# Optimization experiments

Hardware: AMD Instinct MI355X
Metric: run time of the kernel (lower is better)

## Reference

```python
import jax, jax.numpy as jnp
import numpy as np

B, P, O, C = 64, 8732, 32, 81
IMG = 224.0
THRESH = 0.5
NEG_POS = 3.0
ALPHA = 1.0


def cxcy_to_xy(b):
    return jnp.concatenate([b[..., :2] - b[..., 2:] / 2, b[..., :2] + b[..., 2:] / 2], -1)


def xy_to_cxcy(b):
    return jnp.concatenate([(b[..., :2] + b[..., 2:]) / 2, b[..., 2:] - b[..., :2]], -1)


def coco_to_xy(b):  # [x, y, w, h] -> [xmin, ymin, xmax, ymax]
    return jnp.concatenate([b[..., :2], b[..., :2] + b[..., 2:]], -1)


def cxcy_to_gcxgcy(cxcy, priors):  # SSD offset encoding, variances 10 / 5
    g_cxcy = (cxcy[..., :2] - priors[..., :2]) / (priors[..., 2:] / 10.0)
    g_wh = jnp.log(cxcy[..., 2:] / priors[..., 2:]) * 5.0
    return jnp.concatenate([g_cxcy, g_wh], -1)


def pairwise_iou(a, b):  # a: [O,4] xy, b: [P,4] xy -> [O,P]
    lt = jnp.maximum(a[:, None, :2], b[None, :, :2])
    rb = jnp.minimum(a[:, None, 2:], b[None, :, 2:])
    wh = jnp.clip(rb - lt, 0.0)
    inter = wh[..., 0] * wh[..., 1]
    area_a = (a[:, 2] - a[:, 0]) * (a[:, 3] - a[:, 1])
    area_b = (b[:, 2] - b[:, 0]) * (b[:, 3] - b[:, 1])
    return inter / (area_a[:, None] + area_b[None, :] - inter)


def setup_inputs() -> dict:
    key = jax.random.key(0)
    k1, k2, k3, k4, k5, k6, k7 = jax.random.split(key, 7)
    pred_locs = jax.random.normal(k1, (B, P, 4), dtype=jnp.float32)
    pred_scores = jax.random.normal(k2, (B, P, C), dtype=jnp.float32)
    # COCO-format gt boxes [x, y, w, h] in pixel coords, guaranteed inside image
    xy = jax.random.uniform(k3, (B, O, 2), minval=0.0, maxval=IMG * 0.55)
    wh = jax.random.uniform(k4, (B, O, 2), minval=8.0, maxval=IMG * 0.4)
    gt_boxes = jnp.concatenate([xy, wh], -1)
    gt_labels = jax.random.randint(k5, (B, O), 1, C)  # foreground labels 1..C-1
    p_cxcy = jax.random.uniform(k6, (P, 2), minval=0.05, maxval=0.95)
    p_wh = jax.random.uniform(k7, (P, 2), minval=0.05, maxval=0.5)
    priors_cxcy = jnp.concatenate([p_cxcy, p_wh], -1)
    return {"pred_locs": pred_locs, "pred_scores": pred_scores,
            "gt_boxes": gt_boxes, "gt_labels": gt_labels,
            "priors_cxcy": priors_cxcy}


def reference(pred_locs, pred_scores, gt_boxes, gt_labels, priors_cxcy):
    priors_xy = cxcy_to_xy(priors_cxcy)

    def match(boxes_coco, labels):  # one image: [O,4] coco, [O] int
        boxes_xy = coco_to_xy(boxes_coco) / IMG  # normalize to [0,1]
        ov = pairwise_iou(boxes_xy, priors_xy)  # [O, P]
        overlap_for_prior = ov.max(axis=0)       # [P]
        object_for_prior = ov.argmax(axis=0)     # [P]
        prior_for_object = ov.argmax(axis=1)     # [O]
        # force each object to claim its best prior
        object_for_prior = object_for_prior.at[prior_for_object].set(jnp.arange(O))
        overlap_for_prior = overlap_for_prior.at[prior_for_object].set(1.0)
        label_for_prior = labels[object_for_prior]
        label_for_prior = jnp.where(overlap_for_prior < THRESH, 0, label_for_prior)
        true_locs = cxcy_to_gcxgcy(xy_to_cxcy(boxes_xy[object_for_prior]), priors_cxcy)
        return true_locs, label_for_prior

    true_locs, true_classes = jax.vmap(match)(gt_boxes, gt_labels)  # [B,P,4], [B,P]

    positive = true_classes != 0          # [B, P]
    n_pos = positive.sum(axis=1)          # [B]
    n_pos_cl = jnp.maximum(n_pos, 1).astype(jnp.float32)
    n_hard_neg = NEG_POS * n_pos_cl

    # SmoothL1 (beta=1), mean over positive prior coords
    diff = jnp.abs(pred_locs - true_locs)
    sl1 = jnp.where(diff < 1.0, 0.5 * diff * diff, diff - 0.5)  # [B,P,4]
    total_pos = n_pos.sum()
    loc_loss = jnp.where(
        total_pos > 0,
        jnp.where(positive[..., None], sl1, 0.0).sum()
        / jnp.maximum(total_pos * 4, 1).astype(jnp.float32),
        0.0,
    )

    # per-prior cross entropy
    logp = jax.nn.log_softmax(pred_scores, axis=-1)
    ce = -jnp.take_along_axis(logp, true_classes[..., None], axis=-1)[..., 0]  # [B,P]

    conf_pos_sum = jnp.where(positive, ce, 0.0).sum()
    ce_neg = jnp.where(positive, 0.0, ce)
    ce_neg_sorted = -jnp.sort(-ce_neg, axis=1)  # descending per image
    ranks = jnp.arange(P)[None, :]
    hard = ranks < n_hard_neg[:, None]
    conf_hard_neg_sum = jnp.where(hard, ce_neg_sorted, 0.0).sum()

    conf_loss = (conf_hard_neg_sum + conf_pos_sum) / n_pos_cl.sum()
    return conf_loss + ALPHA * loc_loss
```

## Files before the change

### kernel.cpp

```cpp
#include <hip/hip_runtime.h>
#include <cstdint>
#include <cstddef>

#define BB 64
#define PP 8732
#define OO 32
#define CC 81
#define NBM 35
#define TR 64
#define NBC 137

__global__ __launch_bounds__(256) void k_match(
    const float* __restrict__ gt_boxes,
    const float4* __restrict__ priors,
    float* __restrict__ ovl, int* __restrict__ obj,
    unsigned long long* __restrict__ part)
{
    int b = blockIdx.y, blk = blockIdx.x;
    int tid = threadIdx.x;
    int p = blk * 256 + tid;
    bool pv = p < PP;
    __shared__ float bx1[OO], by1[OO], bx2[OO], by2[OO], bar[OO];
    __shared__ float mat[OO][264];
    __shared__ unsigned long long po[OO][8];
    if (tid < OO) {
        const float* g = gt_boxes + ((size_t)b * OO + tid) * 4;
        float x1 = g[0] / 224.0f, y1 = g[1] / 224.0f;
        float x2 = (g[0] + g[2]) / 224.0f, y2 = (g[1] + g[3]) / 224.0f;
        bx1[tid] = x1; by1[tid] = y1; bx2[tid] = x2; by2[tid] = y2;
        bar[tid] = (x2 - x1) * (y2 - y1);
    }
    __syncthreads();
    float4 pr = priors[pv ? p : 0];
    float px1 = pr.x - pr.z * 0.5f, py1 = pr.y - pr.w * 0.5f;
    float px2 = pr.x + pr.z * 0.5f, py2 = pr.y + pr.w * 0.5f;
    float parea = (px2 - px1) * (py2 - py1);
    float best = -1.0f; int bo = 0;
    #pragma unroll
    for (int o = 0; o < OO; ++o) {
        float lx = fmaxf(bx1[o], px1), ly = fmaxf(by1[o], py1);
        float rx = fminf(bx2[o], px2), ry = fminf(by2[o], py2);
        float w = fmaxf(rx - lx, 0.0f), h = fmaxf(ry - ly, 0.0f);
        float inter = w * h;
        float iou = inter / (bar[o] + parea - inter);
        iou = pv ? iou : 0.0f;
        mat[o][tid] = iou;
        if (iou > best) { best = iou; bo = o; }
    }
    if (pv) {
        size_t idx = (size_t)b * PP + p;
        ovl[idx] = best;
        obj[idx] = bo;
    }
    __syncthreads();
    {
        int o = tid >> 3, j = tid & 7;
        float bv = -1.0f; int bt = 0;
        #pragma unroll
        for (int k = 0; k < 32; ++k) {
            int t = j + 8 * k;
            float v = mat[o][t];
            if (v > bv) { bv = v; bt = t; }
        }
        unsigned pg = (unsigned)(blk * 256 + bt);
        po[o][j] = ((unsigned long long)__float_as_uint(bv) << 32)
                 | (unsigned long long)(0xFFFFFFFFu - pg);
    }
    __syncthreads();
    if (tid < OO) {
        unsigned long long m = po[tid][0];
        #pragma unroll
        for (int j = 1; j < 8; ++j) if (po[tid][j] > m) m = po[tid][j];
        part[((size_t)b * NBM + blk) * OO + tid] = m;
    }
}

__global__ void k_force(const unsigned long long* __restrict__ part,
                        float* __restrict__ ovl, int* __restrict__ obj)
{
    int b = blockIdx.x;
    __shared__ int s_pfo[OO];
    int t = threadIdx.x;
    if (t < OO) {
        unsigned long long m = part[((size_t)b * NBM + 0) * OO + t];
        for (int blk = 1; blk < NBM; ++blk) {
            unsigned long long v = part[((size_t)b * NBM + blk) * OO + t];
            if (v > m) m = v;
        }
        s_pfo[t] = (int)(0xFFFFFFFFu - (unsigned)(m & 0xFFFFFFFFull));
    }
    __syncthreads();
    if (t == 0) {
        for (int o = 0; o < OO; ++o) {
            int p = s_pfo[o];
            obj[(size_t)b * PP + p] = o;
            ovl[(size_t)b * PP + p] = 1.0f;
        }
    }
}

__global__ __launch_bounds__(256) void k_ce(
    const float* __restrict__ scores,
    const float4* __restrict__ pred_locs,
    const float* __restrict__ gt_boxes,
    const int* __restrict__ gt_labels,
    const float4* __restrict__ priors,
    const float* __restrict__ ovl, const int* __restrict__ obj,
    float* __restrict__ ceneg,
    float* __restrict__ pp_posce, float* __restrict__ pp_sl1,
    int* __restrict__ pp_np)
{
    int b = blockIdx.y;
    int p0 = blockIdx.x * TR;
    int nrows = PP - p0; if (nrows > TR) nrows = TR;
    int n4 = nrows * CC / 4;
    __shared__ float4 sv4[TR * CC / 4];
    __shared__ int s_lab[TR], s_ob[TR];
    __shared__ float s_posce, s_sl1;
    __shared__ int s_np;
    int tid = threadIdx.x;
    if (tid == 0) { s_posce = 0.f; s_sl1 = 0.f; s_np = 0; }
    if (tid < nrows) {
        size_t idx = (size_t)b * PP + p0 + tid;
        float ov = ovl[idx];
        int ob = obj[idx];
        s_ob[tid] = ob;
        s_lab[tid] = (ov < 0.5f) ? 0 : gt_labels[b * OO + ob];
    }
    const float4* src = (const float4*)(scores + ((size_t)b * PP + p0) * CC);
    for (int i = tid; i < n4; i += 256) sv4[i] = src[i];
    __syncthreads();
    const float* sv = (const float*)sv4;
    int g = tid >> 4, l = tid & 15;
    #pragma unroll
    for (int rr = 0; rr < 4; ++rr) {
        int r = g * 4 + rr;
        if (r >= nrows) break;
        int lab = s_lab[r];
        const float* row = sv + r * CC;
        float se = 0.f, xl = 0.f;
        #pragma unroll
        for (int k = 0; k < 6; ++k) {
            int c = l + 16 * k;
            if (c < CC) {
                float x = row[c];
                se += __expf(x);
                if (c == lab) xl = x;
            }
        }
        #pragma unroll
        for (int s = 8; s >= 1; s >>= 1) {
            se += __shfl_xor(se, s, 16);
            xl += __shfl_xor(xl, s, 16);
        }
        if (l == 0) {
            int p = p0 + r;
            size_t idx = (size_t)b * PP + p;
            float ce = fmaxf(__logf(se) - xl, 0.0f);
            float cn = ce;
            if (lab != 0) {
                cn = 0.f;
                int ob = s_ob[r];
                float4 pl = pred_locs[idx];
                float4 pq = priors[p];
                const float* gg = gt_boxes + ((size_t)b * OO + ob) * 4;
                float x1 = gg[0] / 224.0f, y1 = gg[1] / 224.0f;
                float x2 = (gg[0] + gg[2]) / 224.0f, y2 = (gg[1] + gg[3]) / 224.0f;
                float cx = (x1 + x2) * 0.5f, cy = (y1 + y2) * 0.5f;
                float w = x2 - x1, h = y2 - y1;
                float tx = (cx - pq.x) / (pq.z / 10.0f);
                float ty = (cy - pq.y) / (pq.w / 10.0f);
                float tw = __logf(w / pq.z) * 5.0f;
                float th = __logf(h / pq.w) * 5.0f;
                float d0 = fabsf(pl.x - tx), d1 = fabsf(pl.y - ty);
                float d2 = fabsf(pl.z - tw), d3 = fabsf(pl.w - th);
                float sl = (d0 < 1.f ? 0.5f * d0 * d0 : d0 - 0.5f)
                         + (d1 < 1.f ? 0.5f * d1 * d1 : d1 - 0.5f)
                         + (d2 < 1.f ? 0.5f * d2 * d2 : d2 - 0.5f)
                         + (d3 < 1.f ? 0.5f * d3 * d3 : d3 - 0.5f);
                atomicAdd(&s_posce, ce);
                atomicAdd(&s_sl1, sl);
                atomicAdd(&s_np, 1);
            }
            ceneg[idx] = cn;
        }
    }
    __syncthreads();
    if (tid == 0) {
        int slot = b * NBC + blockIdx.x;
        pp_posce[slot] = s_posce;
        pp_sl1[slot]   = s_sl1;
        pp_np[slot]    = s_np;
    }
}

__global__ __launch_bounds__(512) void k_topk(
    const float* __restrict__ ceneg,
    const float* __restrict__ pp_posce, const float* __restrict__ pp_sl1,
    const int* __restrict__ pp_np,
    float* __restrict__ hard, float* __restrict__ posce_b,
    float* __restrict__ sl1_b, int* __restrict__ n_pos)
{
    int b = blockIdx.x, tid = threadIdx.x;
    __shared__ float4 sv4[PP / 4];
    __shared__ int s_i[8];
    __shared__ float s_f[8], s_f2[8];
    __shared__ int s_bcast;
    float pc = 0.f, sl = 0.f; int np = 0;
    for (int i = tid; i < NBC; i += 512) {
        pc += pp_posce[b * NBC + i];
        sl += pp_sl1[b * NBC + i];
        np += pp_np[b * NBC + i];
    }
    #pragma unroll
    for (int s = 32; s >= 1; s >>= 1) {
        pc += __shfl_xor(pc, s, 64);
        sl += __shfl_xor(sl, s, 64);
        np += __shfl_xor(np, s, 64);
    }
    int wid = tid >> 6;
    if ((tid & 63) == 0) { s_i[wid] = np; s_f[wid] = pc; s_f2[wid] = sl; }
    const float4* src = (const float4*)(ceneg + (size_t)b * PP);
    for (int i = tid; i < PP / 4; i += 512) sv4[i] = src[i];
    __syncthreads();
    if (tid == 0) {
        int n = 0; float fp = 0.f, fs = 0.f;
        #pragma unroll
        for (int k = 0; k < 8; ++k) { n += s_i[k]; fp += s_f[k]; fs += s_f2[k]; }
        n_pos[b] = n; posce_b[b] = fp; sl1_b[b] = fs;
        s_bcast = n;
    }
    __syncthreads();
    np = s_bcast;
    int K = 3 * (np > 1 ? np : 1);
    if (K > PP) K = PP;
    unsigned lo = 0u, hi = 0x7F800000u;
    while (hi - lo > 1u) {
        unsigned mid = (lo + hi) >> 1;
        float t = __uint_as_float(mid);
        int c = 0;
        for (int i = tid; i < PP / 4; i += 512) {
            float4 q = sv4[i];
            c += (q.x >= t) + (q.y >= t) + (q.z >= t) + (q.w >= t);
        }
        #pragma unroll
        for (int s = 32; s >= 1; s >>= 1) c += __shfl_xor(c, s, 64);
        if ((tid & 63) == 0) s_i[wid] = c;
        __syncthreads();
        if (tid == 0) {
            int n = 0;
            #pragma unroll
            for (int k = 0; k < 8; ++k) n += s_i[k];
            s_bcast = n;
        }
        __syncthreads();
        int cnt = s_bcast;
        if (cnt >= K) lo = mid; else hi = mid;
        __syncthreads();
    }
    float vk = __uint_as_float(lo);
    float sm = 0.f; int cg = 0;
    for (int i = tid; i < PP / 4; i += 512) {
        float4 q = sv4[i];
        if (q.x > vk) { sm += q.x; cg++; }
        if (q.y > vk) { sm += q.y; cg++; }
        if (q.z > vk) { sm += q.z; cg++; }
        if (q.w > vk) { sm += q.w; cg++; }
    }
    #pragma unroll
    for (int s = 32; s >= 1; s >>= 1) {
        sm += __shfl_xor(sm, s, 64);
        cg += __shfl_xor(cg, s, 64);
    }
    if ((tid & 63) == 0) { s_f[wid] = sm; s_i[wid] = cg; }
    __syncthreads();
    if (tid == 0) {
        float S = 0.f; int CG = 0;
        #pragma unroll
        for (int k = 0; k < 8; ++k) { S += s_f[k]; CG += s_i[k]; }
        hard[b] = S + (float)(K - CG) * vk;
    }
}

__global__ void k_final(const int* __restrict__ n_pos, const float* __restrict__ hard,
                        const float* __restrict__ posce_b, const float* __restrict__ sl1_b,
                        float* __restrict__ out)
{
    int t = threadIdx.x;
    int np = (t < BB) ? n_pos[t] : 0;
    float h  = (t < BB) ? hard[t] : 0.f;
    float pc = (t < BB) ? posce_b[t] : 0.f;
    float sl = (t < BB) ? sl1_b[t] : 0.f;
    float cl = (t < BB) ? (float)(np > 1 ? np : 1) : 0.f;
    int tp = np; float hs = h; float cls = cl;
    #pragma unroll
    for (int s = 32; s >= 1; s >>= 1) {
        tp  += __shfl_xor(tp, s, 64);
        hs  += __shfl_xor(hs, s, 64);
        cls += __shfl_xor(cls, s, 64);
        pc  += __shfl_xor(pc, s, 64);
        sl  += __shfl_xor(sl, s, 64);
    }
    if (t == 0) {
        float conf = (hs + pc) / cls;
        float loc = 0.f;
        if (tp > 0) {
            int den = tp * 4; if (den < 1) den = 1;
            loc = sl / (float)den;
        }
        out[0] = conf + loc;
    }
}

extern "C" void kernel_launch(void* const* d_in, const int* in_sizes, int n_in,
                              void* d_out, int out_size, void* d_ws, size_t ws_size,
                              hipStream_t stream)
{
    const float* pred_locs   = (const float*)d_in[0];
    const float* pred_scores = (const float*)d_in[1];
    const float* gt_boxes    = (const float*)d_in[2];
    const int*   gt_labels   = (const int*)d_in[3];
    const float* priors      = (const float*)d_in[4];

    char* ws = (char*)d_ws;
    const size_t npf = (size_t)BB * PP;
    size_t off = 0;
    float* ovl   = (float*)(ws + off); off += 4 * npf;
    int*   obj   = (int*)  (ws + off); off += 4 * npf;
    float* ceneg = (float*)(ws + off); off += 4 * npf;
    unsigned long long* part = (unsigned long long*)(ws + off); off += 8 * (size_t)BB * NBM * OO;
    float* pp_posce = (float*)(ws + off); off += 4 * (size_t)BB * NBC;
    float* pp_sl1   = (float*)(ws + off); off += 4 * (size_t)BB * NBC;
    int*   pp_np    = (int*)  (ws + off); off += 4 * (size_t)BB * NBC;
    float* posce_b  = (float*)(ws + off); off += 4 * BB;
    float* sl1_b    = (float*)(ws + off); off += 4 * BB;
    int*   n_pos    = (int*)  (ws + off); off += 4 * BB;
    float* hard     = (float*)(ws + off); off += 4 * BB;

    dim3 gM(NBM, BB);
    k_match<<<gM, 256, 0, stream>>>(gt_boxes, (const float4*)priors, ovl, obj, part);

    k_force<<<BB, 64, 0, stream>>>(part, ovl, obj);

    dim3 gC(NBC, BB);
    k_ce<<<gC, 256, 0, stream>>>(pred_scores, (const float4*)pred_locs, gt_boxes,
                                 gt_labels, (const float4*)priors, ovl, obj,
                                 ceneg, pp_posce, pp_sl1, pp_np);

    k_topk<<<BB, 512, 0, stream>>>(ceneg, pp_posce, pp_sl1, pp_np,
                                   hard, posce_b, sl1_b, n_pos);

    k_final<<<1, 64, 0, stream>>>(n_pos, hard, posce_b, sl1_b, (float*)d_out);
}
```

Baseline: 327.0 us.

## Use 8-ary threshold search in top-k and load CE scores directly to registers

The hard-negative threshold search in k_topk now tests seven thresholds per pass instead of one. This cuts the number of passes over shared memory and block-wide barriers in a kernel that runs only one block per image. k_ce drops its shared-memory staging of the score tile: each 16-lane group loads four rows straight into registers and reduces them together. That removes a block barrier and LDS traffic, but relies on the caches to coalesce global loads of rows that are not aligned to 81 floats.

New measurement: 320.8 us. No clear change (-1.9%).

```diff
diff --git a/kernel.cpp b/kernel.cpp
--- a/kernel.cpp
+++ b/kernel.cpp
@@ -7,8 +7,14 @@
 #define OO 32
 #define CC 81
 #define NBM 35
-#define TR 64
 #define NBC 137
+
+__device__ inline unsigned long long shfl_xor_u64(unsigned long long x, int m) {
+    unsigned lo = (unsigned)x, hi = (unsigned)(x >> 32);
+    lo = (unsigned)__shfl_xor((int)lo, m, 64);
+    hi = (unsigned)__shfl_xor((int)hi, m, 64);
+    return ((unsigned long long)hi << 32) | lo;
+}
 
 __global__ __launch_bounds__(256) void k_match(
     const float* __restrict__ gt_boxes,
@@ -111,61 +117,71 @@
     int* __restrict__ pp_np)
 {
     int b = blockIdx.y;
-    int p0 = blockIdx.x * TR;
-    int nrows = PP - p0; if (nrows > TR) nrows = TR;
-    int n4 = nrows * CC / 4;
-    __shared__ float4 sv4[TR * CC / 4];
-    __shared__ int s_lab[TR], s_ob[TR];
+    int group = threadIdx.x >> 4, lane = threadIdx.x & 15;
+    int pbase = blockIdx.x * 64 + group;
     __shared__ float s_posce, s_sl1;
     __shared__ int s_np;
-    int tid = threadIdx.x;
-    if (tid == 0) { s_posce = 0.f; s_sl1 = 0.f; s_np = 0; }
-    if (tid < nrows) {
-        size_t idx = (size_t)b * PP + p0 + tid;
-        float ov = ovl[idx];
-        int ob = obj[idx];
-        s_ob[tid] = ob;
-        s_lab[tid] = (ov < 0.5f) ? 0 : gt_labels[b * OO + ob];
-    }
-    const float4* src = (const float4*)(scores + ((size_t)b * PP + p0) * CC);
-    for (int i = tid; i < n4; i += 256) sv4[i] = src[i];
-    __syncthreads();
-    const float* sv = (const float*)sv4;
-    int g = tid >> 4, l = tid & 15;
-    #pragma unroll
-    for (int rr = 0; rr < 4; ++rr) {
-        int r = g * 4 + rr;
-        if (r >= nrows) break;
-        int lab = s_lab[r];
-        const float* row = sv + r * CC;
-        float se = 0.f, xl = 0.f;
+    if (threadIdx.x == 0) { s_posce = 0.f; s_sl1 = 0.f; s_np = 0; }
+    __syncthreads();
+    bool vv[4]; size_t ii[4]; int lab[4], ob[4];
+    #pragma unroll
+    for (int q = 0; q < 4; ++q) {
+        int p = pbase + 16 * q;
+        vv[q] = p < PP;
+        ii[q] = (size_t)b * PP + (size_t)(vv[q] ? p : 0);
+        lab[q] = 0; ob[q] = 0;
+        if (vv[q]) {
+            float ov = ovl[ii[q]];
+            ob[q] = obj[ii[q]];
+            lab[q] = (ov < 0.5f) ? 0 : gt_labels[b * OO + ob[q]];
+        }
+    }
+    float a[4][6];
+    #pragma unroll
+    for (int q = 0; q < 4; ++q) {
+        const float* r = scores + ii[q] * CC;
         #pragma unroll
         for (int k = 0; k < 6; ++k) {
-            int c = l + 16 * k;
-            if (c < CC) {
-                float x = row[c];
-                se += __expf(x);
-                if (c == lab) xl = x;
+            int c = lane + 16 * k;
+            a[q][k] = (vv[q] && c < CC) ? r[c] : -INFINITY;
+        }
+    }
+    float se[4] = {0.f, 0.f, 0.f, 0.f}, xl[4] = {0.f, 0.f, 0.f, 0.f};
+    #pragma unroll
+    for (int k = 0; k < 6; ++k) {
+        int c = lane + 16 * k;
+        if (c < CC) {
+            #pragma unroll
+            for (int q = 0; q < 4; ++q) {
+                se[q] += __expf(a[q][k]);
+                if (c == lab[q]) xl[q] = a[q][k];
             }
         }
-        #pragma unroll
-        for (int s = 8; s >= 1; s >>= 1) {
-            se += __shfl_xor(se, s, 16);
-            xl += __shfl_xor(xl, s, 16);
-        }
-        if (l == 0) {
-            int p = p0 + r;
-            size_t idx = (size_t)b * PP + p;
-            float ce = fmaxf(__logf(se) - xl, 0.0f);
+    }
+    #pragma unroll
+    for (int s = 8; s >= 1; s >>= 1) {
+        #pragma unroll
+        for (int q = 0; q < 4; ++q) {
+            se[q] += __shfl_xor(se[q], s, 16);
+            xl[q] += __shfl_xor(xl[q], s, 16);
+        }
+    }
+    if (lane == 0) {
+        #pragma unroll
+        for (int q = 0; q < 4; ++q) {
+            if (!vv[q]) continue;
+            size_t idx = ii[q];
+            int p = pbase + 16 * q;
+            float ce = fmaxf(__logf(se[q]) - xl[q], 0.0f);
             float cn = ce;
-            if (lab != 0) {
+            if (lab[q] != 0) {
                 cn = 0.f;
-                int ob = s_ob[r];
+                int o = ob[q];
                 float4 pl = pred_locs[idx];
                 float4 pq = priors[p];
-                const float* gg = gt_boxes + ((size_t)b * OO + ob) * 4;
-                float x1 = gg[0] / 224.0f, y1 = gg[1] / 224.0f;
-                float x2 = (gg[0] + gg[2]) / 224.0f, y2 = (gg[1] + gg[3]) / 224.0f;
+                const float* g = gt_boxes + ((size_t)b * OO + o) * 4;
+                float x1 = g[0] / 224.0f, y1 = g[1] / 224.0f;
+                float x2 = (g[0] + g[2]) / 224.0f, y2 = (g[1] + g[3]) / 224.0f;
                 float cx = (x1 + x2) * 0.5f, cy = (y1 + y2) * 0.5f;
                 float w = x2 - x1, h = y2 - y1;
                 float tx = (cx - pq.x) / (pq.z / 10.0f);
@@ -186,7 +202,7 @@
         }
     }
     __syncthreads();
-    if (tid == 0) {
+    if (threadIdx.x == 0) {
         int slot = b * NBC + blockIdx.x;
         pp_posce[slot] = s_posce;
         pp_sl1[slot]   = s_sl1;
@@ -202,9 +218,12 @@
     float* __restrict__ sl1_b, int* __restrict__ n_pos)
 {
     int b = blockIdx.x, tid = threadIdx.x;
+    int wave = tid >> 6;
     __shared__ float4 sv4[PP / 4];
     __shared__ int s_i[8];
     __shared__ float s_f[8], s_f2[8];
+    __shared__ int s_cnt[8][8];
+    __shared__ int s_tot[8];
     __shared__ int s_bcast;
     float pc = 0.f, sl = 0.f; int np = 0;
     for (int i = tid; i < NBC; i += 512) {
@@ -218,8 +237,7 @@
         sl += __shfl_xor(sl, s, 64);
         np += __shfl_xor(np, s, 64);
     }
-    int wid = tid >> 6;
-    if ((tid & 63) == 0) { s_i[wid] = np; s_f[wid] = pc; s_f2[wid] = sl; }
+    if ((tid & 63) == 0) { s_i[wave] = np; s_f[wave] = pc; s_f2[wave] = sl; }
     const float4* src = (const float4*)(ceneg + (size_t)b * PP);
     for (int i = tid; i < PP / 4; i += 512) sv4[i] = src[i];
     __syncthreads();
@@ -236,27 +254,44 @@
     if (K > PP) K = PP;
     unsigned lo = 0u, hi = 0x7F800000u;
     while (hi - lo > 1u) {
-        unsigned mid = (lo + hi) >> 1;
-        float t = __uint_as_float(mid);
-        int c = 0;
+        unsigned range = hi - lo;
+        unsigned step = range >> 3; if (step == 0u) step = 1u;
+        unsigned tw[7]; float t[7];
+        #pragma unroll
+        for (int k = 0; k < 7; ++k) {
+            unsigned u = lo + step * (unsigned)(k + 1);
+            if (u > hi) u = hi;
+            tw[k] = u; t[k] = __uint_as_float(u);
+        }
+        int c[7] = {0, 0, 0, 0, 0, 0, 0};
         for (int i = tid; i < PP / 4; i += 512) {
             float4 q = sv4[i];
-            c += (q.x >= t) + (q.y >= t) + (q.z >= t) + (q.w >= t);
-        }
-        #pragma unroll
-        for (int s = 32; s >= 1; s >>= 1) c += __shfl_xor(c, s, 64);
-        if ((tid & 63) == 0) s_i[wid] = c;
+            #pragma unroll
+            for (int k = 0; k < 7; ++k)
+                c[k] += (q.x >= t[k]) + (q.y >= t[k]) + (q.z >= t[k]) + (q.w >= t[k]);
+        }
+        #pragma unroll
+        for (int k = 0; k < 7; ++k)
+            #pragma unroll
+            for (int s = 32; s >= 1; s >>= 1) c[k] += __shfl_xor(c[k], s, 64);
+        if ((tid & 63) == 0) {
+            #pragma unroll
+            for (int k = 0; k < 7; ++k) s_cnt[wave][k] = c[k];
+        }
         __syncthreads();
-        if (tid == 0) {
+        if (tid < 7) {
             int n = 0;
             #pragma unroll
-            for (int k = 0; k < 8; ++k) n += s_i[k];
-            s_bcast = n;
+            for (int w = 0; w < 8; ++w) n += s_cnt[w][tid];
+            s_tot[tid] = n;
         }
         __syncthreads();
-        int cnt = s_bcast;
-        if (cnt >= K) lo = mid; else hi = mid;
-        __syncthreads();
+        int j = -1;
+        #pragma unroll
+        for (int k = 0; k < 7; ++k) if (s_tot[k] >= K) j = k;
+        lo = (j >= 0) ? tw[j] : lo;
+        unsigned nhi = (j < 6) ? tw[j + 1] : hi;
+        hi = (nhi < hi) ? nhi : hi;
     }
     float vk = __uint_as_float(lo);
     float sm = 0.f; int cg = 0;
@@ -272,7 +307,7 @@
         sm += __shfl_xor(sm, s, 64);
         cg += __shfl_xor(cg, s, 64);
     }
-    if ((tid & 63) == 0) { s_f[wid] = sm; s_i[wid] = cg; }
+    if ((tid & 63) == 0) { s_f[wave] = sm; s_i[wave] = cg; }
     __syncthreads();
     if (tid == 0) {
         float S = 0.f; int CG = 0;
```
